# Optimization experiments

Measured on AMD Instinct MI355X. Metric: run time of the kernel, lower is better.

Reference implementation:

```python
import jax, jax.numpy as jnp
import numpy as np

N_NODES = 100000
N_EDGES = 1600000
NODE_DIM = 5
HIDDEN = 64
N_LAYERS = 3


def setup_inputs() -> dict:
    key = jax.random.key(0)
    ks = jax.random.split(key, 12)
    s = 0.1
    return {
        "x": jax.random.normal(ks[0], (N_NODES, NODE_DIM), dtype=jnp.float32),
        "edge_index": jax.random.randint(ks[1], (2, N_EDGES), 0, N_NODES, dtype=jnp.int32),
        # message MLP params per layer (stacked over layers)
        "W1": jax.random.normal(ks[2], (N_LAYERS, 2 * NODE_DIM, HIDDEN), dtype=jnp.float32) * s,
        "b1": jnp.zeros((N_LAYERS, HIDDEN), dtype=jnp.float32),
        "W2": jax.random.normal(ks[3], (N_LAYERS, HIDDEN, NODE_DIM), dtype=jnp.float32) * s,
        "b2": jnp.zeros((N_LAYERS, NODE_DIM), dtype=jnp.float32),
        # update MLP params per layer
        "U1": jax.random.normal(ks[4], (N_LAYERS, 2 * NODE_DIM, HIDDEN), dtype=jnp.float32) * s,
        "bu1": jnp.zeros((N_LAYERS, HIDDEN), dtype=jnp.float32),
        "U2": jax.random.normal(ks[5], (N_LAYERS, HIDDEN, NODE_DIM), dtype=jnp.float32) * s,
        "bu2": jnp.zeros((N_LAYERS, NODE_DIM), dtype=jnp.float32),
        # readout
        "Wr": jax.random.normal(ks[6], (NODE_DIM, NODE_DIM), dtype=jnp.float32) * s,
        "br": jnp.zeros((NODE_DIM,), dtype=jnp.float32),
    }


def reference(x, edge_index, W1, b1, W2, b2, U1, bu1, U2, bu2, Wr, br):
    # PyG convention: messages flow from source j = edge_index[0] to target i = edge_index[1]
    src = edge_index[0]
    dst = edge_index[1]
    n = x.shape[0]
    for l in range(N_LAYERS):
        x_i = x[dst]                                   # [E, d] target features
        x_j = x[src]                                   # [E, d] source features
        msg_in = jnp.concatenate([x_i, x_j], axis=-1)  # [E, 2d]
        msg = jax.nn.relu(msg_in @ W1[l] + b1[l]) @ W2[l] + b2[l]   # [E, d]
        aggr = jax.ops.segment_sum(msg, dst, num_segments=n)        # [N, d] scatter-add at targets
        upd_in = jnp.concatenate([x, aggr], axis=-1)   # [N, 2d]
        upd = jax.nn.relu(upd_in @ U1[l] + bu1[l]) @ U2[l] + bu2[l]  # [N, d]
        x = upd + x                                    # residual (in SkeletonGNN.forward)
    return x @ Wr + br
```

## Files before the change

kernel.cpp:

```cpp
#include <hip/hip_runtime.h>

#define N_NODES 100000
#define N_EDGES 1600000
#define DIM 5
#define HID 64
#define N_LAYERS 3
#define SCAN_BLK 256
#define NBLK ((N_NODES + SCAN_BLK - 1) / SCAN_BLK)


__global__ __launch_bounds__(256) void hist_kernel(
    const int* __restrict__ ei, int* __restrict__ cnt, int* __restrict__ rank)
{
    int e = blockIdx.x * blockDim.x + threadIdx.x;
    if (e >= N_EDGES) return;
    int dst = ei[N_EDGES + e];
    rank[e] = atomicAdd(&cnt[dst], 1);
}

__global__ __launch_bounds__(SCAN_BLK) void scan_part_kernel(
    const int* __restrict__ cnt, int* __restrict__ blk_sum)
{
    __shared__ int s[SCAN_BLK];
    int t = threadIdx.x;
    int i = blockIdx.x * SCAN_BLK + t;
    s[t] = (i < N_NODES) ? cnt[i] : 0;
    __syncthreads();
    for (int off = SCAN_BLK / 2; off > 0; off >>= 1) {
        if (t < off) s[t] += s[t + off];
        __syncthreads();
    }
    if (t == 0) blk_sum[blockIdx.x] = s[0];
}

__global__ __launch_bounds__(512) void scan_blk_kernel(
    const int* __restrict__ blk_sum, int* __restrict__ blk_pref)
{
    __shared__ int s[512];
    int t = threadIdx.x;
    int v = (t < NBLK) ? blk_sum[t] : 0;
    s[t] = v;
    __syncthreads();
    for (int off = 1; off < 512; off <<= 1) {
        int a = (t >= off) ? s[t - off] : 0;
        __syncthreads();
        s[t] += a;
        __syncthreads();
    }
    if (t < NBLK) blk_pref[t] = s[t] - v;
}

__global__ __launch_bounds__(SCAN_BLK) void scan_add_kernel(
    const int* __restrict__ cnt, const int* __restrict__ blk_pref,
    int* __restrict__ row_ptr)
{
    __shared__ int s[SCAN_BLK];
    int t = threadIdx.x;
    int i = blockIdx.x * SCAN_BLK + t;
    int c = (i < N_NODES) ? cnt[i] : 0;
    s[t] = c;
    __syncthreads();
    for (int off = 1; off < SCAN_BLK; off <<= 1) {
        int a = (t >= off) ? s[t - off] : 0;
        __syncthreads();
        s[t] += a;
        __syncthreads();
    }
    if (i < N_NODES) row_ptr[i] = blk_pref[blockIdx.x] + s[t] - c;
    if (i == 0) row_ptr[N_NODES] = N_EDGES;
}

__global__ __launch_bounds__(256) void scatter_kernel(
    const int* __restrict__ ei, const int* __restrict__ rank,
    const int* __restrict__ row_ptr,
    int* __restrict__ ssrc, int* __restrict__ sdst)
{
    int e = blockIdx.x * blockDim.x + threadIdx.x;
    if (e >= N_EDGES) return;
    int src = ei[e];
    int dst = ei[N_EDGES + e];
    int pos = row_ptr[dst] + rank[e];
    ssrc[pos] = src;
    sdst[pos] = dst;
}


__global__ __launch_bounds__(256) void edge_msg_sorted_kernel(
    const float* __restrict__ x,
    const int* __restrict__ ssrc, const int* __restrict__ sdst,
    const float* __restrict__ W1, const float* __restrict__ b1,
    const float* __restrict__ W2, const float* __restrict__ b2,
    float* __restrict__ msg_buf)
{
    int e = blockIdx.x * blockDim.x + threadIdx.x;
    if (e >= N_EDGES) return;
    int src = ssrc[e];
    int dst = sdst[e];

    float in[10];
    const float* xi = x + (long)dst * DIM;
    const float* xj = x + (long)src * DIM;
#pragma unroll
    for (int d = 0; d < DIM; ++d) in[d] = xi[d];
#pragma unroll
    for (int d = 0; d < DIM; ++d) in[DIM + d] = xj[d];

    float msg[DIM];
#pragma unroll
    for (int j = 0; j < DIM; ++j) msg[j] = b2[j];

#pragma unroll 4
    for (int h = 0; h < HID; ++h) {
        float acc = b1[h];
#pragma unroll
        for (int d = 0; d < 10; ++d) acc = fmaf(in[d], W1[d * HID + h], acc);
        acc = fmaxf(acc, 0.0f);
#pragma unroll
        for (int j = 0; j < DIM; ++j) msg[j] = fmaf(acc, W2[h * DIM + j], msg[j]);
    }

    float* mp = msg_buf + (long)e * DIM;
#pragma unroll
    for (int j = 0; j < DIM; ++j) mp[j] = msg[j];
}

template <bool FINAL>
__global__ __launch_bounds__(256) void node_gather_update_kernel(
    const float* __restrict__ x,
    const float* __restrict__ msg_buf,
    const int* __restrict__ row_ptr,
    const float* __restrict__ U1, const float* __restrict__ bu1,
    const float* __restrict__ U2, const float* __restrict__ bu2,
    const float* __restrict__ Wr, const float* __restrict__ br,
    float* __restrict__ xout)
{
    int v = blockIdx.x * blockDim.x + threadIdx.x;
    if (v >= N_NODES) return;

    float in[10];
#pragma unroll
    for (int d = 0; d < DIM; ++d) in[d] = x[(long)v * DIM + d];

    float agg[DIM] = {0.f, 0.f, 0.f, 0.f, 0.f};
    int s = row_ptr[v], epos = row_ptr[v + 1];
    for (int e = s; e < epos; ++e) {
        const float* mp = msg_buf + (long)e * DIM;
#pragma unroll
        for (int j = 0; j < DIM; ++j) agg[j] += mp[j];
    }
#pragma unroll
    for (int d = 0; d < DIM; ++d) in[DIM + d] = agg[d];

    float upd[DIM];
#pragma unroll
    for (int j = 0; j < DIM; ++j) upd[j] = bu2[j];

#pragma unroll 4
    for (int h = 0; h < HID; ++h) {
        float acc = bu1[h];
#pragma unroll
        for (int d = 0; d < 10; ++d) acc = fmaf(in[d], U1[d * HID + h], acc);
        acc = fmaxf(acc, 0.0f);
#pragma unroll
        for (int j = 0; j < DIM; ++j) upd[j] = fmaf(acc, U2[h * DIM + j], upd[j]);
    }

    float xn[DIM];
#pragma unroll
    for (int j = 0; j < DIM; ++j) xn[j] = upd[j] + in[j];

    if (FINAL) {
#pragma unroll
        for (int j = 0; j < DIM; ++j) {
            float o = br[j];
#pragma unroll
            for (int d = 0; d < DIM; ++d) o = fmaf(xn[d], Wr[d * DIM + j], o);
            xout[(long)v * DIM + j] = o;
        }
    } else {
#pragma unroll
        for (int j = 0; j < DIM; ++j) xout[(long)v * DIM + j] = xn[j];
    }
}


__global__ __launch_bounds__(256) void edge_msg_kernel(
    const float* __restrict__ x, const int* __restrict__ ei,
    const float* __restrict__ W1, const float* __restrict__ b1,
    const float* __restrict__ W2, const float* __restrict__ b2,
    float* __restrict__ aggr)
{
    int e = blockIdx.x * blockDim.x + threadIdx.x;
    if (e >= N_EDGES) return;
    int src = ei[e];
    int dst = ei[N_EDGES + e];
    float in[10];
    const float* xi = x + (long)dst * DIM;
    const float* xj = x + (long)src * DIM;
#pragma unroll
    for (int d = 0; d < DIM; ++d) in[d] = xi[d];
#pragma unroll
    for (int d = 0; d < DIM; ++d) in[DIM + d] = xj[d];
    float msg[DIM];
#pragma unroll
    for (int j = 0; j < DIM; ++j) msg[j] = b2[j];
#pragma unroll 4
    for (int h = 0; h < HID; ++h) {
        float acc = b1[h];
#pragma unroll
        for (int d = 0; d < 10; ++d) acc = fmaf(in[d], W1[d * HID + h], acc);
        acc = fmaxf(acc, 0.0f);
#pragma unroll
        for (int j = 0; j < DIM; ++j) msg[j] = fmaf(acc, W2[h * DIM + j], msg[j]);
    }
    float* ap = aggr + (long)dst * DIM;
#pragma unroll
    for (int j = 0; j < DIM; ++j) atomicAdd(ap + j, msg[j]);
}

template <bool FINAL>
__global__ __launch_bounds__(256) void node_upd_kernel(
    const float* __restrict__ x, const float* __restrict__ aggr,
    const float* __restrict__ U1, const float* __restrict__ bu1,
    const float* __restrict__ U2, const float* __restrict__ bu2,
    const float* __restrict__ Wr, const float* __restrict__ br,
    float* __restrict__ xout)
{
    int v = blockIdx.x * blockDim.x + threadIdx.x;
    if (v >= N_NODES) return;
    float in[10];
#pragma unroll
    for (int d = 0; d < DIM; ++d) in[d] = x[(long)v * DIM + d];
#pragma unroll
    for (int d = 0; d < DIM; ++d) in[DIM + d] = aggr[(long)v * DIM + d];
    float upd[DIM];
#pragma unroll
    for (int j = 0; j < DIM; ++j) upd[j] = bu2[j];
#pragma unroll 4
    for (int h = 0; h < HID; ++h) {
        float acc = bu1[h];
#pragma unroll
        for (int d = 0; d < 10; ++d) acc = fmaf(in[d], U1[d * HID + h], acc);
        acc = fmaxf(acc, 0.0f);
#pragma unroll
        for (int j = 0; j < DIM; ++j) upd[j] = fmaf(acc, U2[h * DIM + j], upd[j]);
    }
    float xn[DIM];
#pragma unroll
    for (int j = 0; j < DIM; ++j) xn[j] = upd[j] + in[j];
    if (FINAL) {
#pragma unroll
        for (int j = 0; j < DIM; ++j) {
            float o = br[j];
#pragma unroll
            for (int d = 0; d < DIM; ++d) o = fmaf(xn[d], Wr[d * DIM + j], o);
            xout[(long)v * DIM + j] = o;
        }
    } else {
#pragma unroll
        for (int j = 0; j < DIM; ++j) xout[(long)v * DIM + j] = xn[j];
    }
}


static inline size_t alignup(size_t x) { return (x + 255) & ~(size_t)255; }

extern "C" void kernel_launch(void* const* d_in, const int* in_sizes, int n_in,
                              void* d_out, int out_size, void* d_ws, size_t ws_size,
                              hipStream_t stream) {
    const float* x   = (const float*)d_in[0];
    const int*   ei  = (const int*)d_in[1];
    const float* W1  = (const float*)d_in[2];
    const float* b1  = (const float*)d_in[3];
    const float* W2  = (const float*)d_in[4];
    const float* b2  = (const float*)d_in[5];
    const float* U1  = (const float*)d_in[6];
    const float* bu1 = (const float*)d_in[7];
    const float* U2  = (const float*)d_in[8];
    const float* bu2 = (const float*)d_in[9];
    const float* Wr  = (const float*)d_in[10];
    const float* br  = (const float*)d_in[11];
    float* out = (float*)d_out;

    char* ws = (char*)d_ws;

    size_t o_cnt  = 0;
    size_t o_row  = alignup(o_cnt + (size_t)N_NODES * 4);
    size_t o_bsum = alignup(o_row + (size_t)(N_NODES + 1) * 4);
    size_t o_bpre = alignup(o_bsum + (size_t)NBLK * 4);
    size_t o_ssrc = alignup(o_bpre + (size_t)NBLK * 4);
    size_t o_sdst = alignup(o_ssrc + (size_t)N_EDGES * 4);
    size_t o_xA   = alignup(o_sdst + (size_t)N_EDGES * 4);
    size_t o_xB   = alignup(o_xA + (size_t)N_NODES * DIM * 4);
    size_t o_msg  = alignup(o_xB + (size_t)N_NODES * DIM * 4);
    size_t needed = o_msg + (size_t)N_EDGES * DIM * 4;

    dim3 blk(256);
    dim3 eg((N_EDGES + 255) / 256);
    dim3 ng((N_NODES + 255) / 256);

    if (ws_size < needed) {
        size_t nbytes = (size_t)N_NODES * DIM * sizeof(float);
        float* aggr = (float*)ws;
        float* xA   = (float*)(ws + nbytes);
        float* xB   = (float*)(ws + 2 * nbytes);
        const float* xcur = x;
        for (int l = 0; l < N_LAYERS; ++l) {
            hipMemsetAsync(aggr, 0, nbytes, stream);
            edge_msg_kernel<<<eg, blk, 0, stream>>>(
                xcur, ei, W1 + l * 10 * HID, b1 + l * HID,
                W2 + l * HID * DIM, b2 + l * DIM, aggr);
            if (l < N_LAYERS - 1) {
                float* xn = (l == 0) ? xA : xB;
                node_upd_kernel<false><<<ng, blk, 0, stream>>>(
                    xcur, aggr, U1 + l * 10 * HID, bu1 + l * HID,
                    U2 + l * HID * DIM, bu2 + l * DIM, Wr, br, xn);
                xcur = xn;
            } else {
                node_upd_kernel<true><<<ng, blk, 0, stream>>>(
                    xcur, aggr, U1 + l * 10 * HID, bu1 + l * HID,
                    U2 + l * HID * DIM, bu2 + l * DIM, Wr, br, out);
            }
        }
        return;
    }

    int* cnt      = (int*)(ws + o_cnt);
    int* row_ptr  = (int*)(ws + o_row);
    int* blk_sum  = (int*)(ws + o_bsum);
    int* blk_pref = (int*)(ws + o_bpre);
    int* ssrc     = (int*)(ws + o_ssrc);
    int* sdst     = (int*)(ws + o_sdst);
    float* xA     = (float*)(ws + o_xA);
    float* xB     = (float*)(ws + o_xB);
    float* msgbuf = (float*)(ws + o_msg);
    int* rank     = (int*)(ws + o_msg);

    hipMemsetAsync(cnt, 0, (size_t)N_NODES * 4, stream);
    hist_kernel<<<eg, blk, 0, stream>>>(ei, cnt, rank);
    scan_part_kernel<<<NBLK, SCAN_BLK, 0, stream>>>(cnt, blk_sum);
    scan_blk_kernel<<<1, 512, 0, stream>>>(blk_sum, blk_pref);
    scan_add_kernel<<<NBLK, SCAN_BLK, 0, stream>>>(cnt, blk_pref, row_ptr);
    scatter_kernel<<<eg, blk, 0, stream>>>(ei, rank, row_ptr, ssrc, sdst);

    const float* xcur = x;
    for (int l = 0; l < N_LAYERS; ++l) {
        edge_msg_sorted_kernel<<<eg, blk, 0, stream>>>(
            xcur, ssrc, sdst, W1 + l * 10 * HID, b1 + l * HID,
            W2 + l * HID * DIM, b2 + l * DIM, msgbuf);
        if (l < N_LAYERS - 1) {
            float* xn = (l == 0) ? xA : xB;
            node_gather_update_kernel<false><<<ng, blk, 0, stream>>>(
                xcur, msgbuf, row_ptr, U1 + l * 10 * HID, bu1 + l * HID,
                U2 + l * HID * DIM, bu2 + l * DIM, Wr, br, xn);
            xcur = xn;
        } else {
            node_gather_update_kernel<true><<<ng, blk, 0, stream>>>(
                xcur, msgbuf, row_ptr, U1 + l * 10 * HID, bu1 + l * HID,
                U2 + l * HID * DIM, bu2 + l * DIM, Wr, br, out);
        }
    }
}
```

Before: 410.7 us.

## Pad histogram counters, pack sorted edge pairs as int2, raise MLP unroll

Histogram counters are spread 16 ints apart so atomics on different nodes land on separate cache lines, cutting contention. The sorted src/dst arrays are merged into one int2 array, so the scatter does one store per edge and the message kernel does one 8-byte load. The hidden-loop unroll goes from 4 to 8 in all MLP kernels. The padded counter array needs a 16x larger memset, and the scan kernels now read counters with a strided, uncoalesced pattern.

```diff
diff --git a/kernel.cpp b/kernel.cpp
--- a/kernel.cpp
+++ b/kernel.cpp
@@ -7,6 +7,7 @@
 #define N_LAYERS 3
 #define SCAN_BLK 256
 #define NBLK ((N_NODES + SCAN_BLK - 1) / SCAN_BLK)
+#define CNT_STRIDE 16
 
 
 __global__ __launch_bounds__(256) void hist_kernel(
@@ -15,7 +16,7 @@
     int e = blockIdx.x * blockDim.x + threadIdx.x;
     if (e >= N_EDGES) return;
     int dst = ei[N_EDGES + e];
-    rank[e] = atomicAdd(&cnt[dst], 1);
+    rank[e] = atomicAdd(&cnt[(long)dst * CNT_STRIDE], 1);
 }
 
 __global__ __launch_bounds__(SCAN_BLK) void scan_part_kernel(
@@ -24,7 +25,7 @@
     __shared__ int s[SCAN_BLK];
     int t = threadIdx.x;
     int i = blockIdx.x * SCAN_BLK + t;
-    s[t] = (i < N_NODES) ? cnt[i] : 0;
+    s[t] = (i < N_NODES) ? cnt[(long)i * CNT_STRIDE] : 0;
     __syncthreads();
     for (int off = SCAN_BLK / 2; off > 0; off >>= 1) {
         if (t < off) s[t] += s[t + off];
@@ -57,7 +58,7 @@
     __shared__ int s[SCAN_BLK];
     int t = threadIdx.x;
     int i = blockIdx.x * SCAN_BLK + t;
-    int c = (i < N_NODES) ? cnt[i] : 0;
+    int c = (i < N_NODES) ? cnt[(long)i * CNT_STRIDE] : 0;
     s[t] = c;
     __syncthreads();
     for (int off = 1; off < SCAN_BLK; off <<= 1) {
@@ -70,36 +71,32 @@
     if (i == 0) row_ptr[N_NODES] = N_EDGES;
 }
 
-__global__ __launch_bounds__(256) void scatter_kernel(
+__global__ __launch_bounds__(256) void scatter_pair_kernel(
     const int* __restrict__ ei, const int* __restrict__ rank,
-    const int* __restrict__ row_ptr,
-    int* __restrict__ ssrc, int* __restrict__ sdst)
+    const int* __restrict__ row_ptr, int2* __restrict__ spair)
 {
     int e = blockIdx.x * blockDim.x + threadIdx.x;
     if (e >= N_EDGES) return;
     int src = ei[e];
     int dst = ei[N_EDGES + e];
-    int pos = row_ptr[dst] + rank[e];
-    ssrc[pos] = src;
-    sdst[pos] = dst;
+    spair[row_ptr[dst] + rank[e]] = make_int2(src, dst);
 }
 
 
 __global__ __launch_bounds__(256) void edge_msg_sorted_kernel(
     const float* __restrict__ x,
-    const int* __restrict__ ssrc, const int* __restrict__ sdst,
+    const int2* __restrict__ spair,
     const float* __restrict__ W1, const float* __restrict__ b1,
     const float* __restrict__ W2, const float* __restrict__ b2,
     float* __restrict__ msg_buf)
 {
     int e = blockIdx.x * blockDim.x + threadIdx.x;
     if (e >= N_EDGES) return;
-    int src = ssrc[e];
-    int dst = sdst[e];
+    int2 p = spair[e];
 
     float in[10];
-    const float* xi = x + (long)dst * DIM;
-    const float* xj = x + (long)src * DIM;
+    const float* xi = x + (long)p.y * DIM;
+    const float* xj = x + (long)p.x * DIM;
 #pragma unroll
     for (int d = 0; d < DIM; ++d) in[d] = xi[d];
 #pragma unroll
@@ -109,7 +106,7 @@
 #pragma unroll
     for (int j = 0; j < DIM; ++j) msg[j] = b2[j];
 
-#pragma unroll 4
+#pragma unroll 8
     for (int h = 0; h < HID; ++h) {
         float acc = b1[h];
 #pragma unroll
@@ -155,7 +152,7 @@
 #pragma unroll
     for (int j = 0; j < DIM; ++j) upd[j] = bu2[j];
 
-#pragma unroll 4
+#pragma unroll 8
     for (int h = 0; h < HID; ++h) {
         float acc = bu1[h];
 #pragma unroll
@@ -204,7 +201,7 @@
     float msg[DIM];
 #pragma unroll
     for (int j = 0; j < DIM; ++j) msg[j] = b2[j];
-#pragma unroll 4
+#pragma unroll 8
     for (int h = 0; h < HID; ++h) {
         float acc = b1[h];
 #pragma unroll
@@ -236,7 +233,7 @@
     float upd[DIM];
 #pragma unroll
     for (int j = 0; j < DIM; ++j) upd[j] = bu2[j];
-#pragma unroll 4
+#pragma unroll 8
     for (int h = 0; h < HID; ++h) {
         float acc = bu1[h];
 #pragma unroll
@@ -285,12 +282,11 @@
     char* ws = (char*)d_ws;
 
     size_t o_cnt  = 0;
-    size_t o_row  = alignup(o_cnt + (size_t)N_NODES * 4);
+    size_t o_row  = alignup(o_cnt + (size_t)N_NODES * CNT_STRIDE * 4);
     size_t o_bsum = alignup(o_row + (size_t)(N_NODES + 1) * 4);
     size_t o_bpre = alignup(o_bsum + (size_t)NBLK * 4);
-    size_t o_ssrc = alignup(o_bpre + (size_t)NBLK * 4);
-    size_t o_sdst = alignup(o_ssrc + (size_t)N_EDGES * 4);
-    size_t o_xA   = alignup(o_sdst + (size_t)N_EDGES * 4);
+    size_t o_sp   = alignup(o_bpre + (size_t)NBLK * 4);
+    size_t o_xA   = alignup(o_sp + (size_t)N_EDGES * 8);
     size_t o_xB   = alignup(o_xA + (size_t)N_NODES * DIM * 4);
     size_t o_msg  = alignup(o_xB + (size_t)N_NODES * DIM * 4);
     size_t needed = o_msg + (size_t)N_EDGES * DIM * 4;
@@ -329,24 +325,23 @@
     int* row_ptr  = (int*)(ws + o_row);
     int* blk_sum  = (int*)(ws + o_bsum);
     int* blk_pref = (int*)(ws + o_bpre);
-    int* ssrc     = (int*)(ws + o_ssrc);
-    int* sdst     = (int*)(ws + o_sdst);
+    int2* spair   = (int2*)(ws + o_sp);
     float* xA     = (float*)(ws + o_xA);
     float* xB     = (float*)(ws + o_xB);
     float* msgbuf = (float*)(ws + o_msg);
     int* rank     = (int*)(ws + o_msg);
 
-    hipMemsetAsync(cnt, 0, (size_t)N_NODES * 4, stream);
+    hipMemsetAsync(cnt, 0, (size_t)N_NODES * CNT_STRIDE * 4, stream);
     hist_kernel<<<eg, blk, 0, stream>>>(ei, cnt, rank);
     scan_part_kernel<<<NBLK, SCAN_BLK, 0, stream>>>(cnt, blk_sum);
     scan_blk_kernel<<<1, 512, 0, stream>>>(blk_sum, blk_pref);
     scan_add_kernel<<<NBLK, SCAN_BLK, 0, stream>>>(cnt, blk_pref, row_ptr);
-    scatter_kernel<<<eg, blk, 0, stream>>>(ei, rank, row_ptr, ssrc, sdst);
+    scatter_pair_kernel<<<eg, blk, 0, stream>>>(ei, rank, row_ptr, spair);
 
     const float* xcur = x;
     for (int l = 0; l < N_LAYERS; ++l) {
         edge_msg_sorted_kernel<<<eg, blk, 0, stream>>>(
-            xcur, ssrc, sdst, W1 + l * 10 * HID, b1 + l * HID,
+            xcur, spair, W1 + l * 10 * HID, b1 + l * HID,
             W2 + l * HID * DIM, b2 + l * DIM, msgbuf);
         if (l < N_LAYERS - 1) {
             float* xn = (l == 0) ? xA : xB;
```

After: 387.3 us. -5.7%, faster.
